# Kernel tuning notes

Hardware: AMD Instinct MI355X
Metric: run time of the kernel (lower is better)

## Reference

```python
import jax, jax.numpy as jnp
import numpy as np

N_ATOMS = 100000
N_BONDS = 200000
MAX_NB = 6
ATOM_FDIM = 133
BOND_FDIM = 147
HIDDEN = 300
DEPTH = 3
N_MOLS = 4000


def setup_inputs() -> dict:
    key = jax.random.key(0)
    ks = jax.random.split(key, 10)
    f_atoms = jax.random.normal(ks[0], (N_ATOMS, ATOM_FDIM), dtype=jnp.float32)
    f_bonds = jax.random.normal(ks[1], (N_BONDS, BOND_FDIM), dtype=jnp.float32)
    a2b = jax.random.randint(ks[2], (N_ATOMS, MAX_NB), 0, N_BONDS, dtype=jnp.int32)
    b2a = jax.random.randint(ks[3], (N_BONDS,), 0, N_ATOMS, dtype=jnp.int32)
    b2revb = jax.random.randint(ks[4], (N_BONDS,), 0, N_BONDS, dtype=jnp.int32)
    mol_ids = jnp.sort(jax.random.randint(ks[5], (N_ATOMS,), 0, N_MOLS, dtype=jnp.int32))
    # learned params (W_i, W_h have bias=False; W_o has bias)
    sc = 0.02
    W_i = jax.random.normal(ks[6], (BOND_FDIM, HIDDEN), dtype=jnp.float32) * sc
    W_h = jax.random.normal(ks[7], (HIDDEN, HIDDEN), dtype=jnp.float32) * sc
    W_o = jax.random.normal(ks[8], (ATOM_FDIM + HIDDEN, HIDDEN), dtype=jnp.float32) * sc
    b_o = jax.random.normal(ks[9], (HIDDEN,), dtype=jnp.float32) * sc
    return {"f_atoms": f_atoms, "f_bonds": f_bonds, "a2b": a2b, "b2a": b2a,
            "b2revb": b2revb, "mol_ids": mol_ids, "W_i": W_i, "W_h": W_h,
            "W_o": W_o, "b_o": b_o}


def reference(f_atoms, f_bonds, a2b, b2a, b2revb, mol_ids, W_i, W_h, W_o, b_o):
    # input = W_i(f_bonds); message = relu(input)
    inp = f_bonds @ W_i                              # [n_bonds, H]
    message = jax.nn.relu(inp)
    for _ in range(DEPTH - 1):
        # gather incoming-bond messages per atom and sum over neighbors
        a_message = message[a2b].sum(axis=1)         # [n_atoms, H]
        # directed-bond update: m_b = sum_in(src atom) - reverse message
        message = a_message[b2a] - message[b2revb]   # [n_bonds, H]
        message = jax.nn.relu(inp + message @ W_h)   # dropout p=0 -> identity
    a_message = message[a2b].sum(axis=1)             # [n_atoms, H]
    a_input = jnp.concatenate([f_atoms, a_message], axis=1)
    atom_hiddens = jax.nn.relu(a_input @ W_o + b_o)  # [n_atoms, H]
    # per-molecule mean aggregation (a_scope loop -> segment ops)
    sums = jax.ops.segment_sum(atom_hiddens, mol_ids, num_segments=N_MOLS)
    counts = jax.ops.segment_sum(jnp.ones((atom_hiddens.shape[0], 1), atom_hiddens.dtype),
                                 mol_ids, num_segments=N_MOLS)
    # empty molecules -> cached zero vector
    return jnp.where(counts > 0, sums / jnp.maximum(counts, 1.0), 0.0)
```

## Files before the change

### kernel.cpp

```cpp
#include <hip/hip_runtime.h>

typedef unsigned short bfraw;
typedef __attribute__((ext_vector_type(8))) short short8v;
typedef __attribute__((ext_vector_type(8))) unsigned short ushort8v;
typedef __attribute__((ext_vector_type(4))) float f32x4;

static __device__ __forceinline__ float bf2f(unsigned short u) {
    union { unsigned int i; float f; } c; c.i = ((unsigned int)u) << 16; return c.f;
}
static __device__ __forceinline__ unsigned short f2bf(float f) {
    union { float f; unsigned int i; } c; c.f = f;
    unsigned int r = c.i + 0x7fffu + ((c.i >> 16) & 1u);
    return (unsigned short)(r >> 16);
}
static __device__ __forceinline__ unsigned short brelu(unsigned short u) {
    return (u & 0x8000u) ? (unsigned short)0 : u;
}
static __device__ __forceinline__ f32x4 mfma16(short8v a, short8v b, f32x4 c) {
    return __builtin_amdgcn_mfma_f32_16x16x32_bf16(a, b, c, 0, 0, 0);
}

__global__ __launch_bounds__(64) void k_pack(const float* __restrict__ W, int Krows, int row_off,
                                             bfraw* __restrict__ out) {
    const int b = blockIdx.x;
    const int ks = b / 20, ct = b - ks * 20;
    const int l = threadIdx.x;
    const int n = ct * 16 + (l & 15);
    const int kb = ks * 32 + (l >> 4) * 8;
    short8v pk;
#pragma unroll
    for (int j = 0; j < 8; ++j) {
        int k = kb + j;
        float v = (k < Krows && n < 300) ? W[(row_off + k) * 300 + n] : 0.f;
        pk[j] = (short)f2bf(v);
    }
    *(short8v*)&out[(b * 64 + l) * 8] = pk;
}


__global__ __launch_bounds__(512, 4) void k_in(const float* __restrict__ fb,
                                               const bfraw* __restrict__ Wp,
                                               bfraw* __restrict__ inp,
                                               bfraw* __restrict__ msg) {
    __shared__ short A[64 * 40 * 8];
    const int row0 = blockIdx.x * 64;
    const int tid = threadIdx.x;
    for (int idx = tid; idx < 64 * 20; idx += 512) {
        int r = idx / 20, c = idx - r * 20;
        const int kbase = c * 8;
        const float* src = fb + (long long)(row0 + r) * 147 + kbase;
        short8v pk;
#pragma unroll
        for (int j = 0; j < 8; ++j) {
            float v = (kbase + j < 147) ? src[j] : 0.f;
            pk[j] = (short)f2bf(v);
        }
        *(short8v*)&A[(r * 40 + (c ^ (r & 7))) * 8] = pk;
    }
    __syncthreads();
    const int w = tid >> 6, l = tid & 63;
    const int wr = w >> 2, wc = w & 3;
    const int lr = l & 15, lk = l >> 4, sw = l & 7;
    f32x4 acc[2][5];
#pragma unroll
    for (int ri = 0; ri < 2; ++ri)
#pragma unroll
        for (int i = 0; i < 5; ++i) acc[ri][i] = (f32x4){0.f, 0.f, 0.f, 0.f};
    const short8v* Ald = (const short8v*)A;
#pragma unroll
    for (int ks = 0; ks < 5; ++ks) {
        short8v bfr[2], wv[5];
#pragma unroll
        for (int ri = 0; ri < 2; ++ri)
            bfr[ri] = Ald[((wr * 2 + ri) * 16 + lr) * 40 + ((ks * 4 + lk) ^ sw)];
#pragma unroll
        for (int i = 0; i < 5; ++i)
            wv[i] = *(const short8v*)&Wp[((ks * 20 + wc * 5 + i) * 64 + l) * 8];
#pragma unroll
        for (int ri = 0; ri < 2; ++ri)
#pragma unroll
            for (int i = 0; i < 5; ++i)
                acc[ri][i] = mfma16(wv[i], bfr[ri], acc[ri][i]);
    }
    __syncthreads();
#pragma unroll
    for (int ri = 0; ri < 2; ++ri)
#pragma unroll
        for (int i = 0; i < 5; ++i) {
            const int r = (wr * 2 + ri) * 16 + lr;
            const int c16 = (wc * 5 + i) * 2 + (lk >> 1);
            ushort4 t;
            t.x = f2bf(acc[ri][i][0]); t.y = f2bf(acc[ri][i][1]);
            t.z = f2bf(acc[ri][i][2]); t.w = f2bf(acc[ri][i][3]);
            *(ushort4*)&A[(r * 40 + (c16 ^ (r & 7))) * 8 + (lk & 1) * 4] = t;
        }
    __syncthreads();
    for (int idx = tid; idx < 64 * 38; idx += 512) {
        int r = idx / 38, c = idx - r * 38;
        short8v t = *(const short8v*)&A[(r * 40 + (c ^ (r & 7))) * 8];
        long long o = (long long)(row0 + r) * 304 + c * 8;
        *(short8v*)&inp[o] = t;
        short8v m;
#pragma unroll
        for (int j = 0; j < 8; ++j) m[j] = (short)brelu((unsigned short)t[j]);
        *(short8v*)&msg[o] = m;
    }
}

__global__ __launch_bounds__(256) void k_gather(const bfraw* __restrict__ msg,
                                                const int* __restrict__ a2b,
                                                bfraw* __restrict__ amsg) {
    int gid = blockIdx.x * 256 + threadIdx.x;
    if (gid >= 100000 * 19) return;
    int a = gid / 19, c = gid - a * 19;
    const int* nb = a2b + a * 6;
    float s0[8], s1[8];
#pragma unroll
    for (int e = 0; e < 8; ++e) { s0[e] = 0.f; s1[e] = 0.f; }
#pragma unroll
    for (int j = 0; j < 6; ++j) {
        const long long base = (long long)nb[j] * 304;
        const ushort8v v0 = *(const ushort8v*)&msg[base + c * 8];
        const ushort8v v1 = *(const ushort8v*)&msg[base + (c + 19) * 8];
#pragma unroll
        for (int e = 0; e < 8; ++e) { s0[e] += bf2f(v0[e]); s1[e] += bf2f(v1[e]); }
    }
    short8v o0, o1;
#pragma unroll
    for (int e = 0; e < 8; ++e) { o0[e] = (short)f2bf(s0[e]); o1[e] = (short)f2bf(s1[e]); }
    *(short8v*)&amsg[(long long)a * 304 + c * 8] = o0;
    *(short8v*)&amsg[(long long)a * 304 + (c + 19) * 8] = o1;
}

__global__ __launch_bounds__(512, 4) void k_bond(const bfraw* __restrict__ amsg,
                                                 const bfraw* __restrict__ msg,
                                                 const bfraw* __restrict__ inp,
                                                 const int* __restrict__ b2a,
                                                 const int* __restrict__ b2revb,
                                                 const bfraw* __restrict__ Wp,
                                                 bfraw* __restrict__ out) {
    __shared__ short A[64 * 40 * 8];
    const int row0 = blockIdx.x * 64;
    const int tid = threadIdx.x;
#pragma unroll
    for (int it = 0; it < 5; ++it) {
        int idx = tid + it * 512;
        int r = idx / 40, c = idx - r * 40;
        short8v pk;
        if (c < 38) {
            int b = row0 + r;
            const ushort8v va = *(const ushort8v*)&amsg[(long long)b2a[b] * 304 + c * 8];
            const ushort8v vm = *(const ushort8v*)&msg[(long long)b2revb[b] * 304 + c * 8];
#pragma unroll
            for (int j = 0; j < 8; ++j)
                pk[j] = (short)f2bf(bf2f(va[j]) - bf2f(vm[j]));
        } else {
#pragma unroll
            for (int j = 0; j < 8; ++j) pk[j] = 0;
        }
        *(short8v*)&A[(r * 40 + (c ^ (r & 7))) * 8] = pk;
    }
    __syncthreads();
    const int w = tid >> 6, l = tid & 63;
    const int wr = w >> 2, wc = w & 3;
    const int lr = l & 15, lk = l >> 4, sw = l & 7;
    f32x4 acc[2][5];
#pragma unroll
    for (int ri = 0; ri < 2; ++ri)
#pragma unroll
        for (int i = 0; i < 5; ++i) acc[ri][i] = (f32x4){0.f, 0.f, 0.f, 0.f};
    const short8v* Ald = (const short8v*)A;
#pragma unroll
    for (int ks = 0; ks < 10; ++ks) {
        short8v bfr[2], wv[5];
#pragma unroll
        for (int ri = 0; ri < 2; ++ri)
            bfr[ri] = Ald[((wr * 2 + ri) * 16 + lr) * 40 + ((ks * 4 + lk) ^ sw)];
#pragma unroll
        for (int i = 0; i < 5; ++i)
            wv[i] = *(const short8v*)&Wp[((ks * 20 + wc * 5 + i) * 64 + l) * 8];
#pragma unroll
        for (int ri = 0; ri < 2; ++ri)
#pragma unroll
            for (int i = 0; i < 5; ++i)
                acc[ri][i] = mfma16(wv[i], bfr[ri], acc[ri][i]);
    }
    __syncthreads();
#pragma unroll
    for (int ri = 0; ri < 2; ++ri)
#pragma unroll
        for (int i = 0; i < 5; ++i) {
            const int r = (wr * 2 + ri) * 16 + lr;
            const int c16 = (wc * 5 + i) * 2 + (lk >> 1);
            ushort4 t;
            t.x = f2bf(acc[ri][i][0]); t.y = f2bf(acc[ri][i][1]);
            t.z = f2bf(acc[ri][i][2]); t.w = f2bf(acc[ri][i][3]);
            *(ushort4*)&A[(r * 40 + (c16 ^ (r & 7))) * 8 + (lk & 1) * 4] = t;
        }
    __syncthreads();
    for (int idx = tid; idx < 64 * 38; idx += 512) {
        int r = idx / 38, c = idx - r * 38;
        short8v t = *(const short8v*)&A[(r * 40 + (c ^ (r & 7))) * 8];
        long long o = (long long)(row0 + r) * 304 + c * 8;
        const ushort8v ip = *(const ushort8v*)&inp[o];
        short8v m;
#pragma unroll
        for (int j = 0; j < 8; ++j)
            m[j] = (short)f2bf(fmaxf(bf2f(ip[j]) + bf2f((unsigned short)t[j]), 0.f));
        *(short8v*)&out[o] = m;
    }
}

__global__ __launch_bounds__(512, 4) void k_out(const float* __restrict__ fa,
                                                const bfraw* __restrict__ amsg,
                                                const bfraw* __restrict__ WfP,
                                                const bfraw* __restrict__ WaP,
                                                const float* __restrict__ bo,
                                                bfraw* __restrict__ hid) {
    __shared__ short A[64 * 40 * 8];
    const int row0 = blockIdx.x * 64;
    const int tid = threadIdx.x;
#pragma unroll
    for (int it = 0; it < 5; ++it) {
        int idx = tid + it * 512;
        int r = idx / 40, c = idx - r * 40;
        const int row = row0 + r;
        short8v pk;
        if (c < 38 && row < 100000) {
            const ushort8v v = *(const ushort8v*)&amsg[(long long)row * 304 + c * 8];
#pragma unroll
            for (int j = 0; j < 8; ++j) pk[j] = (short)v[j];
        } else {
#pragma unroll
            for (int j = 0; j < 8; ++j) pk[j] = 0;
        }
        *(short8v*)&A[(r * 40 + (c ^ (r & 7))) * 8] = pk;
    }
    __syncthreads();
    const int w = tid >> 6, l = tid & 63;
    const int wr = w >> 2, wc = w & 3;
    const int lr = l & 15, lk = l >> 4, sw = l & 7;
    f32x4 acc[2][5];
#pragma unroll
    for (int ri = 0; ri < 2; ++ri)
#pragma unroll
        for (int i = 0; i < 5; ++i) acc[ri][i] = (f32x4){0.f, 0.f, 0.f, 0.f};
    const short8v* Ald = (const short8v*)A;
#pragma unroll
    for (int ks = 0; ks < 10; ++ks) {
        short8v bfr[2], wv[5];
#pragma unroll
        for (int ri = 0; ri < 2; ++ri)
            bfr[ri] = Ald[((wr * 2 + ri) * 16 + lr) * 40 + ((ks * 4 + lk) ^ sw)];
#pragma unroll
        for (int i = 0; i < 5; ++i)
            wv[i] = *(const short8v*)&WaP[((ks * 20 + wc * 5 + i) * 64 + l) * 8];
#pragma unroll
        for (int ri = 0; ri < 2; ++ri)
#pragma unroll
            for (int i = 0; i < 5; ++i)
                acc[ri][i] = mfma16(wv[i], bfr[ri], acc[ri][i]);
    }
    __syncthreads();
    for (int idx = tid; idx < 64 * 20; idx += 512) {
        int r = idx / 20, c = idx - r * 20;
        const int row = row0 + r;
        const int kbase = c * 8;
        short8v pk;
        if (row < 100000) {
            const float* src = fa + (long long)row * 133 + kbase;
#pragma unroll
            for (int j = 0; j < 8; ++j) {
                float v = (kbase + j < 133) ? src[j] : 0.f;
                pk[j] = (short)f2bf(v);
            }
        } else {
#pragma unroll
            for (int j = 0; j < 8; ++j) pk[j] = 0;
        }
        *(short8v*)&A[(r * 40 + (c ^ (r & 7))) * 8] = pk;
    }
    __syncthreads();
#pragma unroll
    for (int ks = 0; ks < 5; ++ks) {
        short8v bfr[2], wv[5];
#pragma unroll
        for (int ri = 0; ri < 2; ++ri)
            bfr[ri] = Ald[((wr * 2 + ri) * 16 + lr) * 40 + ((ks * 4 + lk) ^ sw)];
#pragma unroll
        for (int i = 0; i < 5; ++i)
            wv[i] = *(const short8v*)&WfP[((ks * 20 + wc * 5 + i) * 64 + l) * 8];
#pragma unroll
        for (int ri = 0; ri < 2; ++ri)
#pragma unroll
            for (int i = 0; i < 5; ++i)
                acc[ri][i] = mfma16(wv[i], bfr[ri], acc[ri][i]);
    }
    __syncthreads();
#pragma unroll
    for (int ri = 0; ri < 2; ++ri)
#pragma unroll
        for (int i = 0; i < 5; ++i) {
            const int r = (wr * 2 + ri) * 16 + lr;
            const int c16 = (wc * 5 + i) * 2 + (lk >> 1);
            ushort4 t;
            t.x = f2bf(acc[ri][i][0]); t.y = f2bf(acc[ri][i][1]);
            t.z = f2bf(acc[ri][i][2]); t.w = f2bf(acc[ri][i][3]);
            *(ushort4*)&A[(r * 40 + (c16 ^ (r & 7))) * 8 + (lk & 1) * 4] = t;
        }
    __syncthreads();
    for (int idx = tid; idx < 64 * 38; idx += 512) {
        int r = idx / 38, c = idx - r * 38;
        const int row = row0 + r;
        if (row >= 100000) continue;
        short8v t = *(const short8v*)&A[(r * 40 + (c ^ (r & 7))) * 8];
        float4 b0 = *(const float4*)&bo[c * 8];
        float4 b1 = (c < 37) ? *(const float4*)&bo[c * 8 + 4]
                             : make_float4(0.f, 0.f, 0.f, 0.f);
        float bias[8] = {b0.x, b0.y, b0.z, b0.w, b1.x, b1.y, b1.z, b1.w};
        short8v m;
#pragma unroll
        for (int j = 0; j < 8; ++j)
            m[j] = (short)f2bf(fmaxf(bf2f((unsigned short)t[j]) + bias[j], 0.f));
        *(short8v*)&hid[(long long)row * 304 + c * 8] = m;
    }
}

__global__ __launch_bounds__(320) void k_mean(const bfraw* __restrict__ hid,
                                              const int* __restrict__ mol,
                                              float* __restrict__ out) {
    const int m = blockIdx.x;
    const int natoms = 100000;
    int lo = 0, hi = natoms;
    while (lo < hi) { int mid = (lo + hi) >> 1; if (mol[mid] < m) lo = mid + 1; else hi = mid; }
    const int start = lo;
    lo = start; hi = natoms;
    while (lo < hi) { int mid = (lo + hi) >> 1; if (mol[mid] <= m) lo = mid + 1; else hi = mid; }
    const int end = lo;
    const int col = threadIdx.x;
    if (col >= 300) return;
    float s = 0.f;
    for (int a = start; a < end; ++a) s += bf2f(hid[(long long)a * 304 + col]);
    const int n = end - start;
    out[m * 300 + col] = (n > 0) ? (s / (float)n) : 0.f;
}

extern "C" void kernel_launch(void* const* d_in, const int* in_sizes, int n_in,
                              void* d_out, int out_size, void* d_ws, size_t ws_size,
                              hipStream_t stream) {
    const float* f_atoms = (const float*)d_in[0];
    const float* f_bonds = (const float*)d_in[1];
    const int* a2b      = (const int*)d_in[2];
    const int* b2a      = (const int*)d_in[3];
    const int* b2revb   = (const int*)d_in[4];
    const int* mol_ids  = (const int*)d_in[5];
    const float* W_i    = (const float*)d_in[6];
    const float* W_h    = (const float*)d_in[7];
    const float* W_o    = (const float*)d_in[8];
    const float* b_o    = (const float*)d_in[9];
    float* out = (float*)d_out;

    char* wsb = (char*)d_ws;
    bfraw* inp  = (bfraw*)(wsb);
    bfraw* msgA = (bfraw*)(wsb + 121600000ll);
    bfraw* msgB = (bfraw*)(wsb + 243200000ll);
    bfraw* amsg = (bfraw*)(wsb + 364800000ll);
    bfraw* WiP   = (bfraw*)(wsb + 425600000ll);
    bfraw* WhP   = (bfraw*)(wsb + 425702400ll);
    bfraw* WoFaP = (bfraw*)(wsb + 425907200ll);
    bfraw* WoAmP = (bfraw*)(wsb + 426009600ll);

    k_pack<<<100, 64, 0, stream>>>(W_i, 147, 0, WiP);
    k_pack<<<200, 64, 0, stream>>>(W_h, 300, 0, WhP);
    k_pack<<<100, 64, 0, stream>>>(W_o, 133, 0, WoFaP);
    k_pack<<<200, 64, 0, stream>>>(W_o, 300, 133, WoAmP);

    const int nb_blocks = 200000 / 64;
    const int na_blocks = (100000 + 63) / 64;
    const int gather_blocks = (100000 * 19 + 255) / 256;

    k_in<<<nb_blocks, 512, 0, stream>>>(f_bonds, WiP, inp, msgA);

    bfraw* cur = msgA;
    bfraw* nxt = msgB;
    for (int d = 0; d < 2; ++d) {
        k_gather<<<gather_blocks, 256, 0, stream>>>(cur, a2b, amsg);
        k_bond<<<nb_blocks, 512, 0, stream>>>(amsg, cur, inp, b2a, b2revb, WhP, nxt);
        bfraw* t = cur; cur = nxt; nxt = t;
    }
    k_gather<<<gather_blocks, 256, 0, stream>>>(cur, a2b, amsg);

    bfraw* hid = (bfraw*)(wsb + 243200000ll);
    k_out<<<na_blocks, 512, 0, stream>>>(f_atoms, amsg, WoFaP, WoAmP, b_o, hid);
    k_mean<<<4000, 320, 0, stream>>>(hid, mol_ids, out);
}
```

Baseline: 741.2 us.

## Store pre-ReLU messages, apply ReLU on load, fuse final gather into output GEMM

Message buffers now hold pre-activation values, and ReLU is applied when they are consumed. This removes the separate msg write in k_in and the inp-plus-ReLU epilogue read pattern in k_bond. The inp tile in k_bond is prefetched into registers before the gather phase. The last neighbour-sum gather is folded into k_out's A-tile load, which drops one kernel launch and the amsg round trip. k_mean is changed to use vectorised 8-wide loads with an 8-way row split and a shared-memory reduction.

After: 675.1 us. -8.9%, faster.

```diff
diff --git a/kernel.cpp b/kernel.cpp
--- a/kernel.cpp
+++ b/kernel.cpp
@@ -40,8 +40,7 @@
 
 __global__ __launch_bounds__(512, 4) void k_in(const float* __restrict__ fb,
                                                const bfraw* __restrict__ Wp,
-                                               bfraw* __restrict__ inp,
-                                               bfraw* __restrict__ msg) {
+                                               bfraw* __restrict__ inp) {
     __shared__ short A[64 * 40 * 8];
     const int row0 = blockIdx.x * 64;
     const int tid = threadIdx.x;
@@ -98,12 +97,7 @@
     for (int idx = tid; idx < 64 * 38; idx += 512) {
         int r = idx / 38, c = idx - r * 38;
         short8v t = *(const short8v*)&A[(r * 40 + (c ^ (r & 7))) * 8];
-        long long o = (long long)(row0 + r) * 304 + c * 8;
-        *(short8v*)&inp[o] = t;
-        short8v m;
-#pragma unroll
-        for (int j = 0; j < 8; ++j) m[j] = (short)brelu((unsigned short)t[j]);
-        *(short8v*)&msg[o] = m;
+        *(short8v*)&inp[(long long)(row0 + r) * 304 + c * 8] = t;
     }
 }
 
@@ -123,7 +117,10 @@
         const ushort8v v0 = *(const ushort8v*)&msg[base + c * 8];
         const ushort8v v1 = *(const ushort8v*)&msg[base + (c + 19) * 8];
 #pragma unroll
-        for (int e = 0; e < 8; ++e) { s0[e] += bf2f(v0[e]); s1[e] += bf2f(v1[e]); }
+        for (int e = 0; e < 8; ++e) {
+            s0[e] += bf2f(brelu(v0[e]));
+            s1[e] += bf2f(brelu(v1[e]));
+        }
     }
     short8v o0, o1;
 #pragma unroll
@@ -142,6 +139,15 @@
     __shared__ short A[64 * 40 * 8];
     const int row0 = blockIdx.x * 64;
     const int tid = threadIdx.x;
+    ushort8v pf[5];
+#pragma unroll
+    for (int s = 0; s < 5; ++s) {
+        int idx = tid + s * 512;
+        if (idx < 64 * 38) {
+            int r = idx / 38, c = idx - r * 38;
+            pf[s] = *(const ushort8v*)&inp[(long long)(row0 + r) * 304 + c * 8];
+        }
+    }
 #pragma unroll
     for (int it = 0; it < 5; ++it) {
         int idx = tid + it * 512;
@@ -153,7 +159,7 @@
             const ushort8v vm = *(const ushort8v*)&msg[(long long)b2revb[b] * 304 + c * 8];
 #pragma unroll
             for (int j = 0; j < 8; ++j)
-                pk[j] = (short)f2bf(bf2f(va[j]) - bf2f(vm[j]));
+                pk[j] = (short)f2bf(bf2f(va[j]) - bf2f(brelu(vm[j])));
         } else {
 #pragma unroll
             for (int j = 0; j < 8; ++j) pk[j] = 0;
@@ -198,21 +204,24 @@
             *(ushort4*)&A[(r * 40 + (c16 ^ (r & 7))) * 8 + (lk & 1) * 4] = t;
         }
     __syncthreads();
-    for (int idx = tid; idx < 64 * 38; idx += 512) {
-        int r = idx / 38, c = idx - r * 38;
-        short8v t = *(const short8v*)&A[(r * 40 + (c ^ (r & 7))) * 8];
-        long long o = (long long)(row0 + r) * 304 + c * 8;
-        const ushort8v ip = *(const ushort8v*)&inp[o];
-        short8v m;
-#pragma unroll
-        for (int j = 0; j < 8; ++j)
-            m[j] = (short)f2bf(fmaxf(bf2f(ip[j]) + bf2f((unsigned short)t[j]), 0.f));
-        *(short8v*)&out[o] = m;
+#pragma unroll
+    for (int s = 0; s < 5; ++s) {
+        int idx = tid + s * 512;
+        if (idx < 64 * 38) {
+            int r = idx / 38, c = idx - r * 38;
+            short8v t = *(const short8v*)&A[(r * 40 + (c ^ (r & 7))) * 8];
+            short8v m;
+#pragma unroll
+            for (int j = 0; j < 8; ++j)
+                m[j] = (short)f2bf(bf2f(pf[s][j]) + bf2f((unsigned short)t[j]));
+            *(short8v*)&out[(long long)(row0 + r) * 304 + c * 8] = m;
+        }
     }
 }
 
 __global__ __launch_bounds__(512, 4) void k_out(const float* __restrict__ fa,
-                                                const bfraw* __restrict__ amsg,
+                                                const bfraw* __restrict__ msg,
+                                                const int* __restrict__ a2b,
                                                 const bfraw* __restrict__ WfP,
                                                 const bfraw* __restrict__ WaP,
                                                 const float* __restrict__ bo,
@@ -227,9 +236,18 @@
         const int row = row0 + r;
         short8v pk;
         if (c < 38 && row < 100000) {
-            const ushort8v v = *(const ushort8v*)&amsg[(long long)row * 304 + c * 8];
-#pragma unroll
-            for (int j = 0; j < 8; ++j) pk[j] = (short)v[j];
+            const int* nb = a2b + row * 6;
+            float s[8];
+#pragma unroll
+            for (int e = 0; e < 8; ++e) s[e] = 0.f;
+#pragma unroll
+            for (int j = 0; j < 6; ++j) {
+                const ushort8v v = *(const ushort8v*)&msg[(long long)nb[j] * 304 + c * 8];
+#pragma unroll
+                for (int e = 0; e < 8; ++e) s[e] += bf2f(brelu(v[e]));
+            }
+#pragma unroll
+            for (int e = 0; e < 8; ++e) pk[e] = (short)f2bf(s[e]);
         } else {
 #pragma unroll
             for (int j = 0; j < 8; ++j) pk[j] = 0;
@@ -329,6 +347,7 @@
 __global__ __launch_bounds__(320) void k_mean(const bfraw* __restrict__ hid,
                                               const int* __restrict__ mol,
                                               float* __restrict__ out) {
+    __shared__ float red[8][304];
     const int m = blockIdx.x;
     const int natoms = 100000;
     int lo = 0, hi = natoms;
@@ -337,12 +356,28 @@
     lo = start; hi = natoms;
     while (lo < hi) { int mid = (lo + hi) >> 1; if (mol[mid] <= m) lo = mid + 1; else hi = mid; }
     const int end = lo;
-    const int col = threadIdx.x;
-    if (col >= 300) return;
-    float s = 0.f;
-    for (int a = start; a < end; ++a) s += bf2f(hid[(long long)a * 304 + col]);
-    const int n = end - start;
-    out[m * 300 + col] = (n > 0) ? (s / (float)n) : 0.f;
+    const int tid = threadIdx.x;
+    const int p = tid / 38, c = tid - p * 38;
+    if (tid < 304) {
+        float s[8];
+#pragma unroll
+        for (int e = 0; e < 8; ++e) s[e] = 0.f;
+        for (int a = start + p; a < end; a += 8) {
+            const ushort8v v = *(const ushort8v*)&hid[(long long)a * 304 + c * 8];
+#pragma unroll
+            for (int e = 0; e < 8; ++e) s[e] += bf2f(v[e]);
+        }
+#pragma unroll
+        for (int e = 0; e < 8; ++e) red[p][c * 8 + e] = s[e];
+    }
+    __syncthreads();
+    if (tid < 300) {
+        float t = 0.f;
+#pragma unroll
+        for (int p2 = 0; p2 < 8; ++p2) t += red[p2][tid];
+        const int n = end - start;
+        out[m * 300 + tid] = (n > 0) ? (t / (float)n) : 0.f;
+    }
 }
 
 extern "C" void kernel_launch(void* const* d_in, const int* in_sizes, int n_in,
@@ -362,8 +397,8 @@
 
     char* wsb = (char*)d_ws;
     bfraw* inp  = (bfraw*)(wsb);
-    bfraw* msgA = (bfraw*)(wsb + 121600000ll);
-    bfraw* msgB = (bfraw*)(wsb + 243200000ll);
+    bfraw* M1   = (bfraw*)(wsb + 121600000ll);
+    bfraw* M2   = (bfraw*)(wsb + 243200000ll);
     bfraw* amsg = (bfraw*)(wsb + 364800000ll);
     bfraw* WiP   = (bfraw*)(wsb + 425600000ll);
     bfraw* WhP   = (bfraw*)(wsb + 425702400ll);
@@ -379,18 +414,14 @@
     const int na_blocks = (100000 + 63) / 64;
     const int gather_blocks = (100000 * 19 + 255) / 256;
 
-    k_in<<<nb_blocks, 512, 0, stream>>>(f_bonds, WiP, inp, msgA);
-
-    bfraw* cur = msgA;
-    bfraw* nxt = msgB;
-    for (int d = 0; d < 2; ++d) {
-        k_gather<<<gather_blocks, 256, 0, stream>>>(cur, a2b, amsg);
-        k_bond<<<nb_blocks, 512, 0, stream>>>(amsg, cur, inp, b2a, b2revb, WhP, nxt);
-        bfraw* t = cur; cur = nxt; nxt = t;
-    }
-    k_gather<<<gather_blocks, 256, 0, stream>>>(cur, a2b, amsg);
-
-    bfraw* hid = (bfraw*)(wsb + 243200000ll);
-    k_out<<<na_blocks, 512, 0, stream>>>(f_atoms, amsg, WoFaP, WoAmP, b_o, hid);
+    k_in<<<nb_blocks, 512, 0, stream>>>(f_bonds, WiP, inp);
+
+    k_gather<<<gather_blocks, 256, 0, stream>>>(inp, a2b, amsg);
+    k_bond<<<nb_blocks, 512, 0, stream>>>(amsg, inp, inp, b2a, b2revb, WhP, M1);
+    k_gather<<<gather_blocks, 256, 0, stream>>>(M1, a2b, amsg);
+    k_bond<<<nb_blocks, 512, 0, stream>>>(amsg, M1, inp, b2a, b2revb, WhP, M2);
+
+    bfraw* hid = M1;
+    k_out<<<na_blocks, 512, 0, stream>>>(f_atoms, M2, a2b, WoFaP, WoAmP, b_o, hid);
     k_mean<<<4000, 320, 0, stream>>>(hid, mol_ids, out);
 }
```
